# Optimization experiments

Hardware: AMD Instinct MI355X
Metric: run time of the kernel (lower is better)

The kernel has to match this reference:

```python
import jax, jax.numpy as jnp
import numpy as np

DIM = 2048
N_HEADS = 32
N_KV_HEADS = 8
HEAD_DIM = 64
N_REP = N_HEADS // N_KV_HEADS
SEQ = 2048
BATCH = 1


def _llama3_scaled_rope(head_dim, end, base=10000.0, scale_factor=8):
    # matches executorch precompute_freqs_cis with use_scaled=True
    freqs = 1.0 / (base ** (np.arange(0, head_dim, 2)[: head_dim // 2] / head_dim))
    low_freq_factor, high_freq_factor, old_ctx = 1.0, 4.0, 8192.0
    low_wl = old_ctx / low_freq_factor
    high_wl = old_ctx / high_freq_factor
    wavelen = 2.0 * np.pi / freqs
    smooth = (old_ctx / wavelen - low_freq_factor) / (high_freq_factor - low_freq_factor)
    scaled = np.where(
        wavelen < high_wl,
        freqs,
        np.where(wavelen > low_wl, freqs / scale_factor,
                 (1.0 - smooth) * freqs / scale_factor + smooth * freqs),
    )
    t = np.arange(end, dtype=np.float64)
    ang = np.outer(t, scaled)
    return np.cos(ang).astype(np.float32), np.sin(ang).astype(np.float32)


def setup_inputs() -> dict:
    key = jax.random.key(0)
    kx, kq, kk, kv, ko = jax.random.split(key, 5)
    x = jax.random.normal(kx, (BATCH, SEQ, DIM), dtype=jnp.float32)
    sc = 0.02
    wq = jax.random.normal(kq, (N_HEADS * HEAD_DIM, DIM), dtype=jnp.float32) * sc
    wk = jax.random.normal(kk, (N_KV_HEADS * HEAD_DIM, DIM), dtype=jnp.float32) * sc
    wv = jax.random.normal(kv, (N_KV_HEADS * HEAD_DIM, DIM), dtype=jnp.float32) * sc
    wo = jax.random.normal(ko, (N_HEADS * HEAD_DIM, DIM), dtype=jnp.float32).T * sc
    cos, sin = _llama3_scaled_rope(HEAD_DIM, SEQ)
    return {"x": x, "freqs_cos": jnp.asarray(cos), "freqs_sin": jnp.asarray(sin),
            "wq": wq, "wk": wk, "wv": wv, "wo": wo}


def _apply_rotary(x, cos, sin):
    # x: [b, s, h, hd]; cos/sin: [s, hd//2]; interleaved-pair RoPE
    xr = x[..., 0::2]
    xi = x[..., 1::2]
    c = cos[None, :, None, :]
    s = sin[None, :, None, :]
    out_r = xr * c - xi * s
    out_i = xr * s + xi * c
    return jnp.stack([out_r, out_i], axis=-1).reshape(x.shape)


def reference(x, freqs_cos, freqs_sin, wq, wk, wv, wo):
    b, s, _ = x.shape
    q = (x @ wq.T).reshape(b, s, N_HEADS, HEAD_DIM)
    k = (x @ wk.T).reshape(b, s, N_KV_HEADS, HEAD_DIM)
    v = (x @ wv.T).reshape(b, s, N_KV_HEADS, HEAD_DIM)
    q = _apply_rotary(q, freqs_cos, freqs_sin)
    k = _apply_rotary(k, freqs_cos, freqs_sin)
    # [b, h, s, hd]
    q = q.transpose(0, 2, 1, 3)
    k = k.transpose(0, 2, 1, 3)
    v = v.transpose(0, 2, 1, 3)
    # GQA: repeat_interleave over head dim
    k = jnp.repeat(k, N_REP, axis=1)
    v = jnp.repeat(v, N_REP, axis=1)
    scale = 1.0 / jnp.sqrt(jnp.asarray(HEAD_DIM, dtype=x.dtype))
    scores = jnp.einsum("bhqd,bhkd->bhqk", q, k) * scale
    causal = jnp.tril(jnp.ones((s, s), dtype=bool))
    scores = jnp.where(causal[None, None], scores, jnp.finfo(scores.dtype).min)
    attn = jax.nn.softmax(scores, axis=-1)
    y = jnp.einsum("bhqk,bhkd->bhqd", attn, v)
    y = y.transpose(0, 2, 1, 3).reshape(b, s, N_HEADS * HEAD_DIM)
    return y @ wo.T
```

## Files before the change

kernel.cpp:

```cpp
#include <hip/hip_runtime.h>
#include <hip/hip_bf16.h>

typedef __attribute__((ext_vector_type(8))) __bf16 bf16x8;
typedef __attribute__((ext_vector_type(4))) __bf16 bf16x4;
typedef __attribute__((ext_vector_type(4))) float f32x4;

#define DIM 2048
#define SEQ 2048
#define NH 32
#define NKV 8
#define HD 64
#define QKVD 3072
#define KOFF 2048
#define VOFF 2560
#define KVDIM 512

__device__ __forceinline__ void gld16(const __bf16* g, __bf16* l) {
    __builtin_amdgcn_global_load_lds(
        (const __attribute__((address_space(1))) void*)g,
        (__attribute__((address_space(3))) void*)l, 16, 0, 0);
}

__global__ __launch_bounds__(256) void cvt_all(const float* __restrict__ x,
                                               const float* __restrict__ wq,
                                               const float* __restrict__ wk,
                                               const float* __restrict__ wv,
                                               const float* __restrict__ wo,
                                               __bf16* __restrict__ xb,
                                               __bf16* __restrict__ wqkvb,
                                               __bf16* __restrict__ wob) {
    const int i = blockIdx.x * blockDim.x + threadIdx.x;
    const int NX = SEQ * DIM / 4;
    const int NW = DIM * DIM / 4;
    const int NKV4 = KVDIM * DIM / 4;
    const float* src; __bf16* dst; int off;
    if (i < NX)                        { src = x;  dst = xb;    off = i; }
    else if (i < NX + NW)              { src = wq; dst = wqkvb; off = i - NX; }
    else if (i < NX + NW + NKV4)       { src = wk; dst = wqkvb + (size_t)KOFF * DIM; off = i - NX - NW; }
    else if (i < NX + NW + 2 * NKV4)   { src = wv; dst = wqkvb + (size_t)VOFF * DIM; off = i - NX - NW - NKV4; }
    else                               { src = wo; dst = wob;   off = i - NX - NW - 2 * NKV4; }
    float4 v = reinterpret_cast<const float4*>(src)[off];
    bf16x4 o;
    o[0] = (__bf16)v.x; o[1] = (__bf16)v.y; o[2] = (__bf16)v.z; o[3] = (__bf16)v.w;
    reinterpret_cast<bf16x4*>(dst)[off] = o;
}

template <typename OutT, bool ROPE>
__global__ __launch_bounds__(512, 6) void gemm_tn(const __bf16* __restrict__ A,
                                                  const __bf16* __restrict__ B,
                                                  OutT* __restrict__ C,
                                                  int M, int N, int K,
                                                  float scale, int scaleNlim,
                                                  const float* __restrict__ fc,
                                                  const float* __restrict__ fs,
                                                  __bf16* __restrict__ VTout) {
    __shared__ __align__(16) __bf16 As[2][2][128 * 32];
    __shared__ __align__(16) __bf16 Bs[2][2][64 * 32];
    const int tid = threadIdx.x;
    const int lane = tid & 63;
    const int w = tid >> 6;
    const int l15 = lane & 15, lhi = lane >> 4;
    const int mb = blockIdx.y * 128;
    const int nb = blockIdx.x * 64;
    const int wm = (w >> 1) * 32, wn = (w & 1) * 32;

    const int srow = lane >> 2, scol = (lane & 3) * 8;
    const __bf16* gA = A + (size_t)(mb + w * 16 + srow) * K + scol;
    const __bf16* gB = B + (size_t)(nb + (w & 3) * 16 + srow) * K + scol;
    const int bsub = w >> 2;

    auto stage = [&](int kk, int buf) {
#pragma unroll
        for (int s = 0; s < 2; ++s)
            gld16(gA + kk + s * 32, As[buf][s] + w * 512);
        gld16(gB + kk + bsub * 32, Bs[buf][bsub] + (w & 3) * 512);
    };

    stage(0, 0);
    __syncthreads();

    f32x4 acc[2][2] = {};
    int cur = 0;
    for (int kk = 0; kk < K; kk += 64, cur ^= 1) {
        if (kk + 64 < K) stage(kk + 64, cur ^ 1);
#pragma unroll
        for (int s = 0; s < 2; ++s) {
            bf16x8 a[2], b[2];
#pragma unroll
            for (int i = 0; i < 2; ++i)
                a[i] = *reinterpret_cast<const bf16x8*>(&As[cur][s][(wm + i * 16 + l15) * 32 + lhi * 8]);
#pragma unroll
            for (int j = 0; j < 2; ++j)
                b[j] = *reinterpret_cast<const bf16x8*>(&Bs[cur][s][(wn + j * 16 + l15) * 32 + lhi * 8]);
#pragma unroll
            for (int i = 0; i < 2; ++i)
#pragma unroll
                for (int j = 0; j < 2; ++j)
                    acc[i][j] = __builtin_amdgcn_mfma_f32_16x16x32_bf16(a[i], b[j], acc[i][j], 0, 0, 0);
        }
        __syncthreads();
    }

    const bool toVT = ROPE && (VTout != nullptr) && (nb >= VOFF);
    if (toVT) {
#pragma unroll
        for (int i = 0; i < 2; ++i)
#pragma unroll
            for (int j = 0; j < 2; ++j) {
                bf16x4 pv;
#pragma unroll
                for (int r = 0; r < 4; ++r) pv[r] = (__bf16)acc[i][j][r];
                const int colv = nb - VOFF + wn + j * 16 + l15;
                const int row0 = mb + wm + i * 16 + lhi * 4;
                *reinterpret_cast<bf16x4*>(VTout + (size_t)colv * M + row0) = pv;
            }
    } else {
        const float sc = (nb < scaleNlim) ? scale : 1.0f;
        const bool doRope = ROPE && (nb < VOFF);
#pragma unroll
        for (int i = 0; i < 2; ++i)
#pragma unroll
            for (int j = 0; j < 2; ++j)
#pragma unroll
                for (int r = 0; r < 4; ++r) {
                    float v = acc[i][j][r] * sc;
                    if (doRope) {
                        const int col = nb + wn + j * 16 + l15;
                        const int row = mb + wm + i * 16 + lhi * 4 + r;
                        const float vp = __shfl_xor(v, 1);
                        const int fi = (col & 63) >> 1;
                        const float cc = fc[row * 32 + fi];
                        const float ss = fs[row * 32 + fi];
                        v = (col & 1) ? (vp * ss + v * cc) : (v * cc - vp * ss);
                    }
                    C[(size_t)(mb + wm + i * 16 + lhi * 4 + r) * N + nb + wn + j * 16 + l15] = (OutT)v;
                }
    }
}

__global__ __launch_bounds__(256, 4) void attn_kernel(const __bf16* __restrict__ QKV,
                                                      const __bf16* __restrict__ VT,
                                                      __bf16* __restrict__ Y) {
    const int bx = blockIdx.x;
    const int g = bx >> 8;
    const int a = (bx >> 5) & 7;
    const int h = bx & 31;
    const int qt = (g == 0) ? 31 - a : (g == 1) ? a : (g == 2) ? 23 - a : 8 + a;
    const int kvh = h >> 2;
    const int tid = threadIdx.x;
    const int lane = tid & 63;
    const int w = tid >> 6;
    const int l15 = lane & 15, lhi = lane >> 4;

    __shared__ __align__(16) __bf16 Kl[2][64 * 64];
    __shared__ __align__(16) __bf16 Vl[2][64 * 64];
    __shared__ __align__(16) __bf16 Pl[4][16 * 64];

    const __bf16* Qp = QKV + h * HD;
    const __bf16* Kp = QKV + KOFF + kvh * HD;
    const __bf16* Vth = VT + (size_t)(kvh * HD) * SEQ;

    const int sr = lane >> 3;
    const int ksc = ((lane & 7) ^ sr) * 8;
    const int rswz = (l15 & 7);

    auto stage = [&](int jt, int buf) {
        const int kvb = jt * 64;
#pragma unroll
        for (int c = 0; c < 2; ++c) {
            const int row = w * 16 + c * 8;
            gld16(Kp + (size_t)(kvb + row + sr) * QKVD + ksc, &Kl[buf][row * 64]);
            gld16(Vth + (size_t)(row + sr) * SEQ + kvb + ksc, &Vl[buf][row * 64]);
        }
    };

    const int qb = qt * 64;
    const int qrow = qb + w * 16 + l15;

    const __bf16* qptr = Qp + (size_t)qrow * QKVD;
    bf16x8 qf0 = *reinterpret_cast<const bf16x8*>(qptr + lhi * 8);
    bf16x8 qf1 = *reinterpret_cast<const bf16x8*>(qptr + 32 + lhi * 8);

    bf16x8 ones1;
#pragma unroll
    for (int i = 0; i < 8; ++i) ones1[i] = (__bf16)1.0f;

    f32x4 o[4] = {};
    f32x4 oS = {};
    float mrun = -1e30f;

    const int pkey = (l15 & 7) << 1;

    stage(0, 0);
    __syncthreads();

    int cur = 0;
    for (int j = 0; j <= qt; ++j, cur ^= 1) {
        const bool pre = (j < qt);
        if (pre) stage(j + 1, cur ^ 1);

        f32x4 sacc[4];
        __builtin_amdgcn_s_setprio(1);
#pragma unroll
        for (int t = 0; t < 4; ++t) {
            const int rb = (t * 16 + l15) * 64;
            bf16x8 kf0 = *reinterpret_cast<const bf16x8*>(
                &Kl[cur][rb + ((lhi ^ rswz) * 8)]);
            bf16x8 kf1 = *reinterpret_cast<const bf16x8*>(
                &Kl[cur][rb + (((4 + lhi) ^ rswz) * 8)]);
            f32x4 z = {0.f, 0.f, 0.f, 0.f};
            z = __builtin_amdgcn_mfma_f32_16x16x32_bf16(kf0, qf0, z, 0, 0, 0);
            z = __builtin_amdgcn_mfma_f32_16x16x32_bf16(kf1, qf1, z, 0, 0, 0);
            sacc[t] = z;
        }
        __builtin_amdgcn_s_setprio(0);

        if (j == qt) {
#pragma unroll
            for (int t = 0; t < 4; ++t)
#pragma unroll
                for (int r = 0; r < 4; ++r) {
                    const int kv = j * 64 + t * 16 + lhi * 4 + r;
                    if (kv > qrow) sacc[t][r] = -1e30f;
                }
        }

        float mt[4];
#pragma unroll
        for (int t = 0; t < 4; ++t)
            mt[t] = fmaxf(fmaxf(sacc[t][0], sacc[t][1]),
                          fmaxf(sacc[t][2], sacc[t][3]));
        const float pm = fmaxf(fmaxf(mt[0], mt[1]), fmaxf(mt[2], mt[3]));

        if (!__all(pm - mrun <= 8.0f)) {
            float full = pm;
            full = fmaxf(full, __shfl_xor(full, 16));
            full = fmaxf(full, __shfl_xor(full, 32));
            const float mn = fmaxf(mrun, full);
            const float aa = exp2f(mrun - mn);
            mrun = mn;
            float ar[4];
#pragma unroll
            for (int r = 0; r < 4; ++r) ar[r] = __shfl(aa, lhi * 4 + r);
#pragma unroll
            for (int t = 0; t < 4; ++t)
#pragma unroll
                for (int r = 0; r < 4; ++r) o[t][r] *= ar[r];
#pragma unroll
            for (int r = 0; r < 4; ++r) oS[r] *= ar[r];
        }

#pragma unroll
        for (int t = 0; t < 4; ++t) {
            bf16x4 pk;
#pragma unroll
            for (int r = 0; r < 4; ++r)
                pk[r] = (__bf16)exp2f(sacc[t][r] - mrun);
            const int sw = (t * 4 + lhi) ^ pkey;
            *reinterpret_cast<bf16x4*>(&Pl[w][l15 * 64 + sw * 4]) = pk;
        }

        bf16x8 pf0 = *reinterpret_cast<const bf16x8*>(
            &Pl[w][l15 * 64 + (((lhi * 2) ^ pkey) * 4)]);
        bf16x8 pf1 = *reinterpret_cast<const bf16x8*>(
            &Pl[w][l15 * 64 + (((8 + lhi * 2) ^ pkey) * 4)]);
        __builtin_amdgcn_s_setprio(1);
#pragma unroll
        for (int t = 0; t < 4; ++t) {
            const int rb = (t * 16 + l15) * 64;
            bf16x8 vf0 = *reinterpret_cast<const bf16x8*>(
                &Vl[cur][rb + ((lhi ^ rswz) * 8)]);
            bf16x8 vf1 = *reinterpret_cast<const bf16x8*>(
                &Vl[cur][rb + (((4 + lhi) ^ rswz) * 8)]);
            o[t] = __builtin_amdgcn_mfma_f32_16x16x32_bf16(pf0, vf0, o[t], 0, 0, 0);
            o[t] = __builtin_amdgcn_mfma_f32_16x16x32_bf16(pf1, vf1, o[t], 0, 0, 0);
        }
        oS = __builtin_amdgcn_mfma_f32_16x16x32_bf16(pf0, ones1, oS, 0, 0, 0);
        oS = __builtin_amdgcn_mfma_f32_16x16x32_bf16(pf1, ones1, oS, 0, 0, 0);
        __builtin_amdgcn_s_setprio(0);

        __syncthreads();
    }

#pragma unroll
    for (int t = 0; t < 4; ++t)
#pragma unroll
        for (int r = 0; r < 4; ++r) {
            const float val = o[t][r] / oS[r];
            Y[(size_t)(qb + w * 16 + lhi * 4 + r) * DIM + h * HD + t * 16 + l15] =
                (__bf16)val;
        }
}

extern "C" void kernel_launch(void* const* d_in, const int* in_sizes, int n_in,
                              void* d_out, int out_size, void* d_ws, size_t ws_size,
                              hipStream_t stream) {
    const float* x    = (const float*)d_in[0];
    const float* fcos = (const float*)d_in[1];
    const float* fsin = (const float*)d_in[2];
    const float* wq   = (const float*)d_in[3];
    const float* wk   = (const float*)d_in[4];
    const float* wv   = (const float*)d_in[5];
    const float* wo   = (const float*)d_in[6];
    float* out = (float*)d_out;

    __bf16* xb    = (__bf16*)d_ws;
    __bf16* wqkvb = xb + (size_t)SEQ * DIM;
    __bf16* wob   = wqkvb + (size_t)QKVD * DIM;
    __bf16* QKVb  = wob + (size_t)DIM * DIM;
    __bf16* Yb    = QKVb + (size_t)SEQ * QKVD;
    __bf16* VTb   = Yb + (size_t)SEQ * DIM;

    const int ncvt = (SEQ * DIM / 4) + 2 * (DIM * DIM / 4) + 2 * (KVDIM * DIM / 4);
    cvt_all<<<ncvt / 256, 256, 0, stream>>>(x, wq, wk, wv, wo, xb, wqkvb, wob);

    gemm_tn<__bf16, true><<<dim3(QKVD / 64, SEQ / 128), 512, 0, stream>>>(
        xb, wqkvb, QKVb, SEQ, QKVD, DIM, 0.125f * 1.4426950408889634f, KOFF,
        fcos, fsin, VTb);

    attn_kernel<<<dim3(1024), 256, 0, stream>>>(QKVb, VTb, Yb);

    gemm_tn<float, false><<<dim3(DIM / 64, SEQ / 128), 512, 0, stream>>>(
        Yb, wob, out, SEQ, DIM, DIM, 1.0f, 0, nullptr, nullptr, nullptr);
}
```

Baseline: 132.3 us.

## Split attention into 32-row query tiles with 2-wave blocks, drop double buffering

The attention kernel now uses 128-thread blocks, each handling 32 query rows instead of 64, so it launches twice as many blocks. Blocks are ordered longest-first and the old four-way balanced tile interleave is gone. The K/V shared tiles lose their double buffer, and each iteration loads synchronously between two barriers, which shrinks LDS use to allow more resident blocks. The cost is that global loads no longer overlap MFMA work, every K/V tile is loaded twice as often, and causal masking wastes half of the last 64-key tile for even 32-row tiles.

```diff
diff --git a/kernel.cpp b/kernel.cpp
--- a/kernel.cpp
+++ b/kernel.cpp
@@ -138,23 +138,21 @@
     }
 }
 
-__global__ __launch_bounds__(256, 4) void attn_kernel(const __bf16* __restrict__ QKV,
+__global__ __launch_bounds__(128, 4) void attn_kernel(const __bf16* __restrict__ QKV,
                                                       const __bf16* __restrict__ VT,
                                                       __bf16* __restrict__ Y) {
     const int bx = blockIdx.x;
-    const int g = bx >> 8;
-    const int a = (bx >> 5) & 7;
+    const int t = 63 - (bx >> 5);
     const int h = bx & 31;
-    const int qt = (g == 0) ? 31 - a : (g == 1) ? a : (g == 2) ? 23 - a : 8 + a;
     const int kvh = h >> 2;
     const int tid = threadIdx.x;
     const int lane = tid & 63;
     const int w = tid >> 6;
     const int l15 = lane & 15, lhi = lane >> 4;
 
-    __shared__ __align__(16) __bf16 Kl[2][64 * 64];
-    __shared__ __align__(16) __bf16 Vl[2][64 * 64];
-    __shared__ __align__(16) __bf16 Pl[4][16 * 64];
+    __shared__ __align__(16) __bf16 Kl[64 * 64];
+    __shared__ __align__(16) __bf16 Vl[64 * 64];
+    __shared__ __align__(16) __bf16 Pl[2][16 * 64];
 
     const __bf16* Qp = QKV + h * HD;
     const __bf16* Kp = QKV + KOFF + kvh * HD;
@@ -164,17 +162,18 @@
     const int ksc = ((lane & 7) ^ sr) * 8;
     const int rswz = (l15 & 7);
 
-    auto stage = [&](int jt, int buf) {
+    auto stage = [&](int jt) {
         const int kvb = jt * 64;
 #pragma unroll
-        for (int c = 0; c < 2; ++c) {
-            const int row = w * 16 + c * 8;
-            gld16(Kp + (size_t)(kvb + row + sr) * QKVD + ksc, &Kl[buf][row * 64]);
-            gld16(Vth + (size_t)(row + sr) * SEQ + kvb + ksc, &Vl[buf][row * 64]);
+        for (int c = 0; c < 4; ++c) {
+            const int row = w * 32 + c * 8;
+            gld16(Kp + (size_t)(kvb + row + sr) * QKVD + ksc, &Kl[row * 64]);
+            gld16(Vth + (size_t)(row + sr) * SEQ + kvb + ksc, &Vl[row * 64]);
         }
     };
 
-    const int qb = qt * 64;
+    const int qb = t * 32;
+    const int nkt = (t >> 1) + 1;
     const int qrow = qb + w * 16 + l15;
 
     const __bf16* qptr = Qp + (size_t)qrow * QKVD;
@@ -191,45 +190,42 @@
 
     const int pkey = (l15 & 7) << 1;
 
-    stage(0, 0);
-    __syncthreads();
-
-    int cur = 0;
-    for (int j = 0; j <= qt; ++j, cur ^= 1) {
-        const bool pre = (j < qt);
-        if (pre) stage(j + 1, cur ^ 1);
+    for (int j = 0; j < nkt; ++j) {
+        __syncthreads();
+        stage(j);
+        __syncthreads();
 
         f32x4 sacc[4];
         __builtin_amdgcn_s_setprio(1);
 #pragma unroll
-        for (int t = 0; t < 4; ++t) {
-            const int rb = (t * 16 + l15) * 64;
+        for (int tt = 0; tt < 4; ++tt) {
+            const int rb = (tt * 16 + l15) * 64;
             bf16x8 kf0 = *reinterpret_cast<const bf16x8*>(
-                &Kl[cur][rb + ((lhi ^ rswz) * 8)]);
+                &Kl[rb + ((lhi ^ rswz) * 8)]);
             bf16x8 kf1 = *reinterpret_cast<const bf16x8*>(
-                &Kl[cur][rb + (((4 + lhi) ^ rswz) * 8)]);
+                &Kl[rb + (((4 + lhi) ^ rswz) * 8)]);
             f32x4 z = {0.f, 0.f, 0.f, 0.f};
             z = __builtin_amdgcn_mfma_f32_16x16x32_bf16(kf0, qf0, z, 0, 0, 0);
             z = __builtin_amdgcn_mfma_f32_16x16x32_bf16(kf1, qf1, z, 0, 0, 0);
-            sacc[t] = z;
+            sacc[tt] = z;
         }
         __builtin_amdgcn_s_setprio(0);
 
-        if (j == qt) {
-#pragma unroll
-            for (int t = 0; t < 4; ++t)
+        if (j == nkt - 1) {
+#pragma unroll
+            for (int tt = 0; tt < 4; ++tt)
 #pragma unroll
                 for (int r = 0; r < 4; ++r) {
-                    const int kv = j * 64 + t * 16 + lhi * 4 + r;
-                    if (kv > qrow) sacc[t][r] = -1e30f;
+                    const int kv = j * 64 + tt * 16 + lhi * 4 + r;
+                    if (kv > qrow) sacc[tt][r] = -1e30f;
                 }
         }
 
         float mt[4];
 #pragma unroll
-        for (int t = 0; t < 4; ++t)
-            mt[t] = fmaxf(fmaxf(sacc[t][0], sacc[t][1]),
-                          fmaxf(sacc[t][2], sacc[t][3]));
+        for (int tt = 0; tt < 4; ++tt)
+            mt[tt] = fmaxf(fmaxf(sacc[tt][0], sacc[tt][1]),
+                           fmaxf(sacc[tt][2], sacc[tt][3]));
         const float pm = fmaxf(fmaxf(mt[0], mt[1]), fmaxf(mt[2], mt[3]));
 
         if (!__all(pm - mrun <= 8.0f)) {
@@ -243,20 +239,20 @@
 #pragma unroll
             for (int r = 0; r < 4; ++r) ar[r] = __shfl(aa, lhi * 4 + r);
 #pragma unroll
-            for (int t = 0; t < 4; ++t)
-#pragma unroll
-                for (int r = 0; r < 4; ++r) o[t][r] *= ar[r];
+            for (int tt = 0; tt < 4; ++tt)
+#pragma unroll
+                for (int r = 0; r < 4; ++r) o[tt][r] *= ar[r];
 #pragma unroll
             for (int r = 0; r < 4; ++r) oS[r] *= ar[r];
         }
 
 #pragma unroll
-        for (int t = 0; t < 4; ++t) {
+        for (int tt = 0; tt < 4; ++tt) {
             bf16x4 pk;
 #pragma unroll
             for (int r = 0; r < 4; ++r)
-                pk[r] = (__bf16)exp2f(sacc[t][r] - mrun);
-            const int sw = (t * 4 + lhi) ^ pkey;
+                pk[r] = (__bf16)exp2f(sacc[tt][r] - mrun);
+            const int sw = (tt * 4 + lhi) ^ pkey;
             *reinterpret_cast<bf16x4*>(&Pl[w][l15 * 64 + sw * 4]) = pk;
         }
 
@@ -266,28 +262,26 @@
             &Pl[w][l15 * 64 + (((8 + lhi * 2) ^ pkey) * 4)]);
         __builtin_amdgcn_s_setprio(1);
 #pragma unroll
-        for (int t = 0; t < 4; ++t) {
-            const int rb = (t * 16 + l15) * 64;
+        for (int tt = 0; tt < 4; ++tt) {
+            const int rb = (tt * 16 + l15) * 64;
             bf16x8 vf0 = *reinterpret_cast<const bf16x8*>(
-                &Vl[cur][rb + ((lhi ^ rswz) * 8)]);
+                &Vl[rb + ((lhi ^ rswz) * 8)]);
             bf16x8 vf1 = *reinterpret_cast<const bf16x8*>(
-                &Vl[cur][rb + (((4 + lhi) ^ rswz) * 8)]);
-            o[t] = __builtin_amdgcn_mfma_f32_16x16x32_bf16(pf0, vf0, o[t], 0, 0, 0);
-            o[t] = __builtin_amdgcn_mfma_f32_16x16x32_bf16(pf1, vf1, o[t], 0, 0, 0);
+                &Vl[rb + (((4 + lhi) ^ rswz) * 8)]);
+            o[tt] = __builtin_amdgcn_mfma_f32_16x16x32_bf16(pf0, vf0, o[tt], 0, 0, 0);
+            o[tt] = __builtin_amdgcn_mfma_f32_16x16x32_bf16(pf1, vf1, o[tt], 0, 0, 0);
         }
         oS = __builtin_amdgcn_mfma_f32_16x16x32_bf16(pf0, ones1, oS, 0, 0, 0);
         oS = __builtin_amdgcn_mfma_f32_16x16x32_bf16(pf1, ones1, oS, 0, 0, 0);
         __builtin_amdgcn_s_setprio(0);
-
-        __syncthreads();
     }
 
 #pragma unroll
-    for (int t = 0; t < 4; ++t)
+    for (int tt = 0; tt < 4; ++tt)
 #pragma unroll
         for (int r = 0; r < 4; ++r) {
-            const float val = o[t][r] / oS[r];
-            Y[(size_t)(qb + w * 16 + lhi * 4 + r) * DIM + h * HD + t * 16 + l15] =
+            const float val = o[tt][r] / oS[r];
+            Y[(size_t)(qb + w * 16 + lhi * 4 + r) * DIM + h * HD + tt * 16 + l15] =
                 (__bf16)val;
         }
 }
@@ -318,7 +312,7 @@
         xb, wqkvb, QKVb, SEQ, QKVD, DIM, 0.125f * 1.4426950408889634f, KOFF,
         fcos, fsin, VTb);
 
-    attn_kernel<<<dim3(1024), 256, 0, stream>>>(QKVb, VTb, Yb);
+    attn_kernel<<<dim3(2048), 128, 0, stream>>>(QKVb, VTb, Yb);
 
     gemm_tn<float, false><<<dim3(DIM / 64, SEQ / 128), 512, 0, stream>>>(
         Yb, wob, out, SEQ, DIM, DIM, 1.0f, 0, nullptr, nullptr, nullptr);
```

Result: slower. 137.5 us (+3.9%).
